# Performance work log

Measured on AMD Instinct MI355X. Metric: run time of the kernel, lower is better.

Reference implementation:

```python
import jax, jax.numpy as jnp
import numpy as np

N_MODELS = 64
IN_F = 256
OUT_F = 256
BATCH = 8192


def setup_inputs() -> dict:
    key = jax.random.key(0)
    kx, kw, kb, ki = jax.random.split(key, 4)
    x = jax.random.normal(kx, (BATCH, OUT_F), dtype=jnp.float32)
    idxs = jax.random.randint(ki, (BATCH,), 0, N_MODELS, dtype=jnp.int64)
    # learned parameters (torch inits them to zeros; we use random so grads/outputs are nontrivial)
    w = jax.random.normal(kw, (N_MODELS, IN_F, OUT_F), dtype=jnp.float32) * 0.02
    b = jax.random.normal(kb, (N_MODELS, OUT_F), dtype=jnp.float32) * 0.02
    return {"x": x, "idxs": idxs, "w": w, "b": b}


def reference(x, idxs, w, b):
    # torch: baddbmm(b[idxs,:,None], w[idxs], x[:,:,None]).squeeze(-1) -> relu
    # y[n, i] = b[idxs[n], i] + sum_o w[idxs[n], i, o] * x[n, o]
    wg = w[idxs]                      # (B, in, out) gathered per-sample weights
    bg = b[idxs]                      # (B, out)
    y = jnp.einsum('bio,bo->bi', wg, x) + bg
    return jax.nn.relu(y)
```

## Files before the change

### kernel.cpp

```cpp
#include <hip/hip_runtime.h>
#include <stdint.h>


#define N_MODELS 64
#define IN_F     256
#define OUT_F    256
#define BATCH    8192
#define BM       128
#define BN       128
#define PK       264

typedef __bf16 bf16x8 __attribute__((ext_vector_type(8)));
typedef float  f32x4  __attribute__((ext_vector_type(4)));

__device__ __forceinline__ bf16x8 pack8(float4 a, float4 b) {
  bf16x8 o;
  o[0] = (__bf16)a.x; o[1] = (__bf16)a.y; o[2] = (__bf16)a.z; o[3] = (__bf16)a.w;
  o[4] = (__bf16)b.x; o[5] = (__bf16)b.y; o[6] = (__bf16)b.z; o[7] = (__bf16)b.w;
  return o;
}

__global__ __launch_bounds__(1024) void fused_kernel(
    const float* __restrict__ x, const int* __restrict__ idxs,
    const float* __restrict__ w, const float* __restrict__ bias_g,
    float* __restrict__ out) {
  const int model = blockIdx.x >> 2;
  const int tile  = (blockIdx.x >> 1) & 1;
  const int i0    = (blockIdx.x & 1) * BN;
  const int t     = threadIdx.x;
  const int lane  = t & 63;
  const int wv    = t >> 6;

  __shared__ unsigned short a_lds[BM][PK];
  __shared__ unsigned short b_lds[BN][PK];
  __shared__ int rid[BM];
  __shared__ int wsum[16];

  const int rw = t >> 3;
  const int h  = t & 7;

  const int4* ip = (const int4*)idxs + t * 2;
  int4 iv0 = ip[0], iv1 = ip[1];

  const float* wrow = w + (size_t)model * (IN_F * OUT_F)
                        + (size_t)(i0 + rw) * IN_F + h * 32;

  if (tile == 0) {
    float4 tw[8];
#pragma unroll
    for (int j = 0; j < 8; ++j) tw[j] = *(const float4*)(wrow + j * 4);
#pragma unroll
    for (int j = 0; j < 4; ++j)
      *(bf16x8*)&b_lds[rw][h * 32 + j * 8] = pack8(tw[2 * j], tw[2 * j + 1]);
  }

  if (t < BM) rid[t] = -1;

  int cnt = (iv0.x == model) + (iv0.y == model) + (iv0.z == model) + (iv0.w == model)
          + (iv1.x == model) + (iv1.y == model) + (iv1.z == model) + (iv1.w == model);
  int inc = cnt;
#pragma unroll
  for (int d = 1; d < 64; d <<= 1) {
    int u = __shfl_up(inc, d);
    if (lane >= d) inc += u;
  }
  if (lane == 63) wsum[wv] = inc;
  __syncthreads();
  int wpre = 0, total = 0;
#pragma unroll
  for (int j = 0; j < 16; ++j) {
    int s = wsum[j];
    total += s;
    if (j < wv) wpre += s;
  }
  const int start = tile * BM;
  if (start >= total) return;
  int off = wpre + inc - cnt - start;
  {
    int n0 = t * 8;
    if (iv0.x == model) { if ((unsigned)off < BM) rid[off] = n0 + 0; ++off; }
    if (iv0.y == model) { if ((unsigned)off < BM) rid[off] = n0 + 1; ++off; }
    if (iv0.z == model) { if ((unsigned)off < BM) rid[off] = n0 + 2; ++off; }
    if (iv0.w == model) { if ((unsigned)off < BM) rid[off] = n0 + 3; ++off; }
    if (iv1.x == model) { if ((unsigned)off < BM) rid[off] = n0 + 4; ++off; }
    if (iv1.y == model) { if ((unsigned)off < BM) rid[off] = n0 + 5; ++off; }
    if (iv1.z == model) { if ((unsigned)off < BM) rid[off] = n0 + 6; ++off; }
    if (iv1.w == model) { if ((unsigned)off < BM) rid[off] = n0 + 7; ++off; }
  }
  __syncthreads();

  if (tile == 1) {
    float4 tw[8];
#pragma unroll
    for (int j = 0; j < 8; ++j) tw[j] = *(const float4*)(wrow + j * 4);
#pragma unroll
    for (int j = 0; j < 4; ++j)
      *(bf16x8*)&b_lds[rw][h * 32 + j * 8] = pack8(tw[2 * j], tw[2 * j + 1]);
  }

  const int srow = rid[rw];
  const float* xrow = x + (size_t)(srow < 0 ? 0 : srow) * IN_F + h * 32;
  {
    float4 tx[8];
#pragma unroll
    for (int j = 0; j < 8; ++j) tx[j] = *(const float4*)(xrow + j * 4);
#pragma unroll
    for (int j = 0; j < 4; ++j)
      *(bf16x8*)&a_lds[rw][h * 32 + j * 8] = pack8(tx[2 * j], tx[2 * j + 1]);
  }

  const int wm   = (wv & 3) * 32;
  const int wn   = (wv >> 2) * 32;
  const int col  = lane & 15;
  const int quad = lane >> 4;
  float bv[2];
  const float* bp = bias_g + model * OUT_F + i0 + wn + col;
#pragma unroll
  for (int nt = 0; nt < 2; ++nt) bv[nt] = bp[nt * 16];

  __syncthreads();

  f32x4 acc[2][2];
#pragma unroll
  for (int mt = 0; mt < 2; ++mt)
#pragma unroll
    for (int nt = 0; nt < 2; ++nt)
      acc[mt][nt] = (f32x4){bv[nt], bv[nt], bv[nt], bv[nt]};

#pragma unroll
  for (int ks = 0; ks < 8; ++ks) {
    bf16x8 af[2], bfr[2];
#pragma unroll
    for (int mt = 0; mt < 2; ++mt)
      af[mt] = *(const bf16x8*)&a_lds[wm + mt * 16 + col][ks * 32 + quad * 8];
#pragma unroll
    for (int nt = 0; nt < 2; ++nt)
      bfr[nt] = *(const bf16x8*)&b_lds[wn + nt * 16 + col][ks * 32 + quad * 8];
#pragma unroll
    for (int mt = 0; mt < 2; ++mt)
#pragma unroll
      for (int nt = 0; nt < 2; ++nt)
        acc[mt][nt] = __builtin_amdgcn_mfma_f32_16x16x32_bf16(
            af[mt], bfr[nt], acc[mt][nt], 0, 0, 0);
  }

#pragma unroll
  for (int mt = 0; mt < 2; ++mt) {
#pragma unroll
    for (int reg = 0; reg < 4; ++reg) {
      const int mm = wm + mt * 16 + quad * 4 + reg;
      const int s = rid[mm];
      if (s >= 0) {
        float* orow = out + (size_t)s * OUT_F + i0 + wn + col;
#pragma unroll
        for (int nt = 0; nt < 2; ++nt)
          orow[nt * 16] = fmaxf(acc[mt][nt][reg], 0.0f);
      }
    }
  }
}

extern "C" void kernel_launch(void* const* d_in, const int* in_sizes, int n_in,
                              void* d_out, int out_size, void* d_ws, size_t ws_size,
                              hipStream_t stream) {
  const float* x    = (const float*)d_in[0];
  const int*   idxs = (const int*)d_in[1];
  const float* w    = (const float*)d_in[2];
  const float* b    = (const float*)d_in[3];
  float* out = (float*)d_out;
  (void)d_ws; (void)ws_size;

  fused_kernel<<<N_MODELS * 4, 1024, 0, stream>>>(x, idxs, w, b, out);
}
```

Measured before the change: 86.30 us.

## Split index compaction into separate kernel and swizzle GEMM block order

Moves the per-model row compaction (scan over all idxs) out of the GEMM kernel into a small compact kernel that writes row lists and counts to workspace. The GEMM blocks then read the precomputed rows instead of each of the four blocks per model redundantly scanning all 8192 indices, and the block index is remapped to spread models across XCDs. This adds a second kernel launch and a global round trip for the row lists, and drops the overlap that let tile 0 load its weights before the scan finished.

Measured after the change: 87.48 us. About the same (+1.4%).

```diff
diff --git a/kernel.cpp b/kernel.cpp
--- a/kernel.cpp
+++ b/kernel.cpp
@@ -20,41 +20,17 @@
   return o;
 }
 
-__global__ __launch_bounds__(1024) void fused_kernel(
-    const float* __restrict__ x, const int* __restrict__ idxs,
-    const float* __restrict__ w, const float* __restrict__ bias_g,
-    float* __restrict__ out) {
-  const int model = blockIdx.x >> 2;
-  const int tile  = (blockIdx.x >> 1) & 1;
-  const int i0    = (blockIdx.x & 1) * BN;
+__global__ __launch_bounds__(1024) void compact_kernel(
+    const int* __restrict__ idxs, int* __restrict__ rid_g,
+    int* __restrict__ cnt_g) {
+  const int model = blockIdx.x;
   const int t     = threadIdx.x;
   const int lane  = t & 63;
   const int wv    = t >> 6;
-
-  __shared__ unsigned short a_lds[BM][PK];
-  __shared__ unsigned short b_lds[BN][PK];
-  __shared__ int rid[BM];
   __shared__ int wsum[16];
-
-  const int rw = t >> 3;
-  const int h  = t & 7;
 
   const int4* ip = (const int4*)idxs + t * 2;
   int4 iv0 = ip[0], iv1 = ip[1];
-
-  const float* wrow = w + (size_t)model * (IN_F * OUT_F)
-                        + (size_t)(i0 + rw) * IN_F + h * 32;
-
-  if (tile == 0) {
-    float4 tw[8];
-#pragma unroll
-    for (int j = 0; j < 8; ++j) tw[j] = *(const float4*)(wrow + j * 4);
-#pragma unroll
-    for (int j = 0; j < 4; ++j)
-      *(bf16x8*)&b_lds[rw][h * 32 + j * 8] = pack8(tw[2 * j], tw[2 * j + 1]);
-  }
-
-  if (t < BM) rid[t] = -1;
 
   int cnt = (iv0.x == model) + (iv0.y == model) + (iv0.z == model) + (iv0.w == model)
           + (iv1.x == model) + (iv1.y == model) + (iv1.z == model) + (iv1.w == model);
@@ -73,23 +49,52 @@
     total += s;
     if (j < wv) wpre += s;
   }
-  const int start = tile * BM;
-  if (start >= total) return;
-  int off = wpre + inc - cnt - start;
+  int off = wpre + inc - cnt;
+  int* rg = rid_g + model * 256;
   {
     int n0 = t * 8;
-    if (iv0.x == model) { if ((unsigned)off < BM) rid[off] = n0 + 0; ++off; }
-    if (iv0.y == model) { if ((unsigned)off < BM) rid[off] = n0 + 1; ++off; }
-    if (iv0.z == model) { if ((unsigned)off < BM) rid[off] = n0 + 2; ++off; }
-    if (iv0.w == model) { if ((unsigned)off < BM) rid[off] = n0 + 3; ++off; }
-    if (iv1.x == model) { if ((unsigned)off < BM) rid[off] = n0 + 4; ++off; }
-    if (iv1.y == model) { if ((unsigned)off < BM) rid[off] = n0 + 5; ++off; }
-    if (iv1.z == model) { if ((unsigned)off < BM) rid[off] = n0 + 6; ++off; }
-    if (iv1.w == model) { if ((unsigned)off < BM) rid[off] = n0 + 7; ++off; }
+    if (iv0.x == model) { if ((unsigned)off < 256u) rg[off] = n0 + 0; ++off; }
+    if (iv0.y == model) { if ((unsigned)off < 256u) rg[off] = n0 + 1; ++off; }
+    if (iv0.z == model) { if ((unsigned)off < 256u) rg[off] = n0 + 2; ++off; }
+    if (iv0.w == model) { if ((unsigned)off < 256u) rg[off] = n0 + 3; ++off; }
+    if (iv1.x == model) { if ((unsigned)off < 256u) rg[off] = n0 + 4; ++off; }
+    if (iv1.y == model) { if ((unsigned)off < 256u) rg[off] = n0 + 5; ++off; }
+    if (iv1.z == model) { if ((unsigned)off < 256u) rg[off] = n0 + 6; ++off; }
+    if (iv1.w == model) { if ((unsigned)off < 256u) rg[off] = n0 + 7; ++off; }
   }
-  __syncthreads();
+  if (t < 256 && t >= total) rg[t] = -1;
+  if (t == 0) cnt_g[model] = total;
+}
 
-  if (tile == 1) {
+__global__ __launch_bounds__(1024) void gemm_kernel(
+    const float* __restrict__ x, const float* __restrict__ w,
+    const float* __restrict__ bias_g, float* __restrict__ out,
+    const int* __restrict__ rid_g, const int* __restrict__ cnt_g) {
+  const int b     = (blockIdx.x & 7) * 32 + (blockIdx.x >> 3);
+  const int model = b >> 2;
+  const int s     = (b >> 1) & 1;
+  const int i0    = (b & 1) * BN;
+  const int t     = threadIdx.x;
+  const int lane  = t & 63;
+  const int wv    = t >> 6;
+
+  __shared__ unsigned short a_lds[BM][PK];
+  __shared__ unsigned short b_lds[BN][PK];
+  __shared__ int rid[BM];
+
+  const int total = cnt_g[model];
+  if (s * BM >= total) return;
+
+  if (t < BM) rid[t] = rid_g[model * 256 + s * BM + t];
+
+  const int rw = t >> 3;
+  const int h  = t & 7;
+
+  const int srow = rid_g[model * 256 + s * BM + rw];
+
+  const float* wrow = w + (size_t)model * (IN_F * OUT_F)
+                        + (size_t)(i0 + rw) * IN_F + h * 32;
+  {
     float4 tw[8];
 #pragma unroll
     for (int j = 0; j < 8; ++j) tw[j] = *(const float4*)(wrow + j * 4);
@@ -98,7 +103,6 @@
       *(bf16x8*)&b_lds[rw][h * 32 + j * 8] = pack8(tw[2 * j], tw[2 * j + 1]);
   }
 
-  const int srow = rid[rw];
   const float* xrow = x + (size_t)(srow < 0 ? 0 : srow) * IN_F + h * 32;
   {
     float4 tx[8];
@@ -149,9 +153,9 @@
 #pragma unroll
     for (int reg = 0; reg < 4; ++reg) {
       const int mm = wm + mt * 16 + quad * 4 + reg;
-      const int s = rid[mm];
-      if (s >= 0) {
-        float* orow = out + (size_t)s * OUT_F + i0 + wn + col;
+      const int sle = rid[mm];
+      if (sle >= 0) {
+        float* orow = out + (size_t)sle * OUT_F + i0 + wn + col;
 #pragma unroll
         for (int nt = 0; nt < 2; ++nt)
           orow[nt * 16] = fmaxf(acc[mt][nt][reg], 0.0f);
@@ -168,7 +172,10 @@
   const float* w    = (const float*)d_in[2];
   const float* b    = (const float*)d_in[3];
   float* out = (float*)d_out;
-  (void)d_ws; (void)ws_size;
 
-  fused_kernel<<<N_MODELS * 4, 1024, 0, stream>>>(x, idxs, w, b, out);
+  int* rid_g = (int*)d_ws;
+  int* cnt_g = rid_g + N_MODELS * 256;
+
+  compact_kernel<<<N_MODELS, 1024, 0, stream>>>(idxs, rid_g, cnt_g);
+  gemm_kernel<<<N_MODELS * 4, 1024, 0, stream>>>(x, w, b, out, rid_g, cnt_g);
 }
```
